# Performance work log

Hardware: AMD Instinct MI355X
Metric: run time of the kernel (lower is better)

## Reference

```python
import jax, jax.numpy as jnp
import numpy as np
import math

K = 32          # knn neighbors
NN = 32         # num_neighbor (kernel columns)
MAP = 32        # map_size
GROUP = 4
IN_C = 64
OUT_C = 64
EPS = 1e-5
TOPK = 3        # neighbors kept per kernel column in topkmax


def knn_idx(xc, k):
    # xc: [B,N,3]; returns indices of k nearest points (self included first)
    sq = -jnp.sum(xc * xc, axis=-1, keepdims=True)            # [B,N,1]
    pair = sq + 2.0 * jnp.einsum('bnd,bmd->bnm', xc, xc) + jnp.swapaxes(sq, 1, 2)
    return jax.lax.top_k(pair, k)[1]                          # [B,N,k]


def topkmax(p):
    # p: [M,k,NN]; keep top-TOPK along neighbor axis (dim=1), softmax over it
    pt = jnp.swapaxes(p, 1, 2)                                # [M,NN,k]
    thr = jax.lax.top_k(pt, TOPK)[0][..., -1:]
    pt = jnp.where(pt >= thr, pt, -1e10)
    return jnp.swapaxes(jax.nn.softmax(pt, axis=-1), 1, 2)


def setup_inputs() -> dict:
    key = jax.random.key(0)
    ks = jax.random.split(key, 8)
    B, N = 8, 2048
    in_c_x = IN_C // 2
    F = IN_C + in_c_x                                         # 96
    return {
        'x': jax.random.normal(ks[0], (B, 3, N), jnp.float32),
        'feature': jax.random.normal(ks[1], (B, IN_C, N), jnp.float32),
        'B_mat': jax.random.normal(ks[2], (7, MAP), jnp.float32),
        'kernels': jax.random.normal(ks[3], (3, NN), jnp.float32),
        'mlp_w': jax.random.normal(ks[4], (in_c_x, 2 * MAP), jnp.float32) * 0.1,
        'mlp_b': jnp.zeros((in_c_x,), jnp.float32),
        'conv_w': jax.random.normal(ks[5], (OUT_C, F * NN), jnp.float32) * 0.02,
        'conv_b': jnp.zeros((OUT_C,), jnp.float32),
        'bn_gamma': jnp.ones((OUT_C,), jnp.float32),
        'bn_beta': jnp.zeros((OUT_C,), jnp.float32),
    }


def reference(x, feature, B_mat, kernels, mlp_w, mlp_b, conv_w, conv_b, bn_gamma, bn_beta):
    bsz, in_c, n = feature.shape
    in_c_x = in_c // 2
    F = in_c + in_c_x
    M = bsz * n

    xc = jnp.swapaxes(x, 1, 2)                                # [B,N,3]
    idx = knn_idx(xc, K)                                      # [B,N,K]
    bix = jnp.arange(bsz)[:, None, None]

    x_neighs = xc[bix, idx].reshape(M, K, 3)                  # gather coords
    x_rep = jnp.broadcast_to(x_neighs[:, :1, :], x_neighs.shape)
    x_rel = x_neighs - x_rep
    x_dis = jnp.linalg.norm(x_rel, axis=-1, keepdims=True)

    # random Fourier features of [center, relative, distance]
    ff = (2.0 * math.pi) * jnp.concatenate([x_rep, x_rel, x_dis], -1) @ B_mat  # [M,K,MAP]
    ff = jnp.concatenate([jnp.sin(ff), jnp.cos(ff)], -1)                        # [M,K,2*MAP]
    x_feats = jnp.einsum('mki,oi->mok', ff, mlp_w) + mlp_b[None, :, None]       # [M,in_c_x,K]

    fN = jnp.swapaxes(feature, 1, 2)                          # [B,N,C]
    feats = fN[bix, idx].reshape(M, K, in_c)                  # gather features
    feats = jnp.swapaxes(feats, 1, 2)                         # [M,C,K]
    feats = jnp.concatenate([feats, x_feats], axis=1)         # [M,F,K]

    one_pad = jnp.zeros((K, NN), feature.dtype).at[0, 0].set(1.0)
    perm = topkmax(jnp.einsum('mkd,dn->mkn', x_rel, kernels) + one_pad)  # [M,K,NN]

    # group channel shuffle (F > 3 + in_c_x holds for in_c=64)
    feats = feats.reshape(M, GROUP, F // GROUP, K).transpose(0, 2, 1, 3).reshape(M, F, K)
    feats = jnp.einsum('mfk,mkn->mfn', feats, perm).reshape(M, F * NN)

    out = (feats @ conv_w.T + conv_b).reshape(bsz, n, -1)
    out = jnp.swapaxes(out, 1, 2)                             # [B,out_c,N]

    # BatchNorm1d, training-mode batch statistics over (B,N)
    mean = out.mean(axis=(0, 2), keepdims=True)
    var = out.var(axis=(0, 2), keepdims=True)
    return bn_gamma[None, :, None] * (out - mean) / jnp.sqrt(var + EPS) + bn_beta[None, :, None]
```

## Files before the change

kernel.cpp:

```cpp
#include <hip/hip_runtime.h>
#include <hip/hip_bf16.h>
#include <math.h>

#define NPTS 2048
#define NBATCH 8
#define MTOT (NBATCH*NPTS)
#define KROW 4096
#define OUTC 64

using bf16x8 = __attribute__((ext_vector_type(8))) short;
using f32x4  = __attribute__((ext_vector_type(4))) float;

__device__ __forceinline__ unsigned short f2bf(float f) {
    unsigned u = __float_as_uint(f);
    unsigned r = u + 0x7FFFu + ((u >> 16) & 1u);
    return (unsigned short)(r >> 16);
}
__device__ __forceinline__ unsigned pk2bf(float lo, float hi) {
    __hip_bfloat162 h2 = __float22bfloat162_rn(make_float2(lo, hi));
    return *reinterpret_cast<unsigned*>(&h2);
}

__device__ __forceinline__ unsigned wave_max_u32(unsigned v) {
    int x = (int)v, t;
    t = __builtin_amdgcn_update_dpp(x, x, 0x111, 0xF, 0xF, false); x = ((unsigned)t > (unsigned)x) ? t : x;
    t = __builtin_amdgcn_update_dpp(x, x, 0x112, 0xF, 0xF, false); x = ((unsigned)t > (unsigned)x) ? t : x;
    t = __builtin_amdgcn_update_dpp(x, x, 0x114, 0xF, 0xF, false); x = ((unsigned)t > (unsigned)x) ? t : x;
    t = __builtin_amdgcn_update_dpp(x, x, 0x118, 0xF, 0xF, false); x = ((unsigned)t > (unsigned)x) ? t : x;
    t = __builtin_amdgcn_update_dpp(x, x, 0x142, 0xa, 0xF, false); x = ((unsigned)t > (unsigned)x) ? t : x;
    t = __builtin_amdgcn_update_dpp(x, x, 0x143, 0xc, 0xF, false); x = ((unsigned)t > (unsigned)x) ? t : x;
    return (unsigned)__builtin_amdgcn_readlane(x, 63);
}

__global__ __launch_bounds__(512, 4) void knn_kernel(const float* __restrict__ x,
                                                     int* __restrict__ idxout) {
    __shared__ float4 ps[NPTS];
    int t = threadIdx.x;
    int b = blockIdx.x / (NPTS / 8);
    int grp = blockIdx.x % (NPTS / 8);
    const float* xb = x + (size_t)b * 3 * NPTS;
    for (int i = t; i < NPTS; i += 512) {
        float vx = xb[i], vy = xb[NPTS + i], vz = xb[2 * NPTS + i];
        ps[i] = make_float4(vx, vy, vz, -((vx * vx + vy * vy) + vz * vz));
    }
    __syncthreads();
    int wave = t >> 6, lane = t & 63;
    int n = grp * 8 + wave;
    float4 pc = ps[n];
    float cx = pc.x, cy = pc.y, cz = pc.z;
    float sqn = pc.w;
    float cx2 = 2.0f * cx, cy2 = 2.0f * cy, cz2 = 2.0f * cz;

    unsigned key[32];
#pragma unroll
    for (int j = 0; j < 32; j++) {
        int cand = j * 64 + lane;
        float4 q = ps[cand];
        float v = sqn + q.w;
        v = fmaf(cx2, q.x, v);
        v = fmaf(cy2, q.y, v);
        v = fmaf(cz2, q.z, v);
        unsigned u = __float_as_uint(v);
        unsigned ord = u ^ ((u >> 31) ? 0xFFFFFFFFu : 0x80000000u);
        key[j] = (ord & 0xFFFFFFE0u) | (unsigned)j;
    }
#pragma unroll
    for (int k = 2; k <= 32; k <<= 1) {
#pragma unroll
        for (int j = k >> 1; j >= 1; j >>= 1) {
#pragma unroll
            for (int i = 0; i < 32; i++) {
                int l2 = i ^ j;
                if (l2 > i) {
                    unsigned a = key[i], bb = key[l2];
                    unsigned hi = a > bb ? a : bb, lo = a > bb ? bb : a;
                    if ((i & k) == 0) { key[i] = hi; key[l2] = lo; }
                    else              { key[i] = lo; key[l2] = hi; }
                }
            }
        }
    }
    int sg = 0;
    for (int r = 0; r < 40; r++) {
        unsigned m = wave_max_u32(key[0]);
        unsigned long long ball = __ballot(key[0] == m);
        int bl = __ffsll(ball) - 1;
        int gidx = (int)(m & 31u) * 64 + bl;
        if (lane == r) sg = gidx;
        bool won = (lane == bl);
#pragma unroll
        for (int i = 0; i < 11; i++) key[i] = won ? key[i + 1] : key[i];
        key[11] = won ? 0u : key[11];
    }
    double cxd = (double)cx, cyd = (double)cy, czd = (double)cz;
    double sqnd = -((cxd * cxd + cyd * cyd) + czd * czd);
    double v; int oid;
    if (lane < 40) {
        float4 qq = ps[sg];
        double mx = (double)qq.x, my = (double)qq.y, mz = (double)qq.z;
        double dot = (cxd * mx + cyd * my) + czd * mz;
        double sqm = -((mx * mx + my * my) + mz * mz);
        v = (sqnd + 2.0 * dot) + sqm;
        oid = sg;
    } else {
        v = -1.0e300; oid = (1 << 28) + lane;
    }
#pragma unroll
    for (int k = 2; k <= 64; k <<= 1) {
#pragma unroll
        for (int j = k >> 1; j >= 1; j >>= 1) {
            double ov = __shfl_xor(v, j);
            int oi = __shfl_xor(oid, j);
            bool amLow = (lane & j) == 0;
            bool asc = (lane & k) == 0;
            bool gt = (ov > v) || (ov == v && oi < oid);
            bool ga = gt != amLow;
            bool take = asc ? ga : !ga;
            if (take) { v = ov; oid = oi; }
        }
    }
    if (lane >= 32) idxout[((size_t)b * NPTS + n) * 32 + (63 - lane)] = oid;
}

__global__ __launch_bounds__(256) void transpose_kernel(const float* __restrict__ feat,
                                                        unsigned short* __restrict__ fTb) {
    __shared__ float tile[64][65];
    int b = blockIdx.x / 32;
    int n0 = (blockIdx.x % 32) * 64;
    int t = threadIdx.x;
    int nt = t % 64, cg = t / 64;
    for (int cc = 0; cc < 16; cc++) {
        int c2 = cg * 16 + cc;
        tile[c2][nt] = feat[((size_t)b * 64 + c2) * NPTS + n0 + nt];
    }
    __syncthreads();
    int c2 = t % 64, ng = t / 64;
    for (int nn2 = 0; nn2 < 16; nn2++) {
        int n = ng * 16 + nn2;
        fTb[((size_t)b * NPTS + n0 + n) * 64 + c2] = f2bf(tile[c2][n]);
    }
}

__global__ __launch_bounds__(256) void wprep2_kernel(
    const float* __restrict__ cw, const float* __restrict__ mlpw,
    const float* __restrict__ mb, const float* __restrict__ cb,
    unsigned short* __restrict__ WtT, float* __restrict__ cbw) {
    int oc = blockIdx.x;
    int t = threadIdx.x;
    for (int i = t; i < 2048; i += 256) {
        int f = i >> 5, col = i & 31;
        int r = (f % 24) * 4 + f / 24;
        WtT[(size_t)oc * KROW + i] = f2bf(cw[(size_t)oc * 3072 + r * 32 + col]);
    }
    for (int i = t; i < 2048; i += 256) {
        int j = i >> 5, col = i & 31;
        float s = 0.f;
        for (int o2 = 0; o2 < 32; o2++) {
            int f = 64 + o2;
            int r = (f % 24) * 4 + f / 24;
            s = fmaf(mlpw[o2 * 64 + j], cw[(size_t)oc * 3072 + r * 32 + col], s);
        }
        WtT[(size_t)oc * KROW + 2048 + i] = f2bf(s);
    }
    if (t == 0) {
        float s = cb[oc];
        for (int o2 = 0; o2 < 32; o2++) {
            int f = 64 + o2;
            int r = (f % 24) * 4 + f / 24;
            float rowsum = 0.f;
            for (int col = 0; col < 32; col++) rowsum += cw[(size_t)oc * 3072 + r * 32 + col];
            s = fmaf(mb[o2], rowsum, s);
        }
        cbw[oc] = s;
    }
}

__global__ void kprep_kernel(const float* __restrict__ ker, double* __restrict__ kerd) {
    int i = threadIdx.x;
    if (i < 96) kerd[i] = (double)ker[i];
}

__global__ __launch_bounds__(256) void perm_kernel(
    const float* __restrict__ x, const int* __restrict__ idx,
    const double* __restrict__ kerd, unsigned short* __restrict__ PTws) {
    int t = threadIdx.x;
    int wv = t >> 6, l = t & 63;
    int c = l & 31;
    int cbase = l & 32;
    int m = blockIdx.x * 8 + wv * 2 + (l >> 5);
    int b = m >> 11;
    int ik = idx[(size_t)m * 32 + c];
    const float* xb = x + (size_t)b * 3 * NPTS;
    float nx0 = xb[ik], ny0 = xb[NPTS + ik], nz0 = xb[2 * NPTS + ik];
    float cx = __shfl(nx0, cbase), cy = __shfl(ny0, cbase), cz = __shfl(nz0, cbase);
    double rxd = (double)nx0 - (double)cx;
    double ryd = (double)ny0 - (double)cy;
    double rzd = (double)nz0 - (double)cz;
    double ck0 = kerd[c], ck1 = kerd[32 + c], ck2 = kerd[64 + c];

    double pd[32];
#pragma unroll
    for (int kk = 0; kk < 32; kk++) {
        double bx = __shfl(rxd, cbase + kk);
        double by = __shfl(ryd, cbase + kk);
        double bz = __shfl(rzd, cbase + kk);
        pd[kk] = bx * ck0 + by * ck1 + bz * ck2;
    }
    if (c == 0) pd[0] += 1.0;

    double m1 = -1.0e300, m2 = -1.0e300, m3 = -1.0e300;
#pragma unroll
    for (int kk = 0; kk < 32; kk++) {
        double v = pd[kk];
        double t2 = fmin(v, m1);
        double t3 = fmin(v, m2);
        m1 = fmax(m1, v);
        m2 = fmax(m2, t2);
        m3 = fmax(m3, t3);
    }
    float pv[32];
    float ssum = 0.f;
#pragma unroll
    for (int kk = 0; kk < 32; kk++) {
        float e = (pd[kk] >= m3) ? __expf((float)(pd[kk] - m1)) : 0.f;
        pv[kk] = e; ssum += e;
    }
    float rs = 1.f / ssum;
#pragma unroll
    for (int kk = 0; kk < 32; kk++) pv[kk] *= rs;

    unsigned w[16];
#pragma unroll
    for (int i = 0; i < 16; i++)
        w[i] = pk2bf(pv[2 * i], pv[2 * i + 1]);
    size_t obase = (size_t)m * 1024 + (size_t)c * 32;
    *(uint4*)&PTws[obase]      = make_uint4(w[0], w[1], w[2], w[3]);
    *(uint4*)&PTws[obase + 8]  = make_uint4(w[4], w[5], w[6], w[7]);
    *(uint4*)&PTws[obase + 16] = make_uint4(w[8], w[9], w[10], w[11]);
    *(uint4*)&PTws[obase + 24] = make_uint4(w[12], w[13], w[14], w[15]);
}

__global__ __launch_bounds__(256) void point3_kernel(
    const float* __restrict__ x, const unsigned short* __restrict__ fTb,
    const int* __restrict__ idx, const float* __restrict__ Bm,
    const unsigned short* __restrict__ PTws, unsigned short* __restrict__ Aof,
    int m_base, int m_count) {
    __shared__ __align__(16) unsigned short lds2[4 * 2560];
    int t = threadIdx.x;
    int wv = t >> 6, l = t & 63;
    int k = l & 31, h = l >> 5;
    unsigned short* G2 = lds2 + wv * 2560;
    int lr = l & 15, lq = l >> 4;
    int gw = blockIdx.x * 4 + wv;
    int nw = gridDim.x * 4;

    for (int mi = gw; mi < m_count; mi += nw) {
        int m = m_base + mi;
        int b = m >> 11;
        int ik = idx[(size_t)m * 32 + k];
        const float* xb = x + (size_t)b * 3 * NPTS;
        float nx0 = xb[ik], ny0 = xb[NPTS + ik], nz0 = xb[2 * NPTS + ik];
        const unsigned short* fr = fTb + (((size_t)b * NPTS + ik) * 64 + h * 32);
        uint4 f0 = *(const uint4*)fr;
        uint4 f1 = *(const uint4*)(fr + 8);
        uint4 f2 = *(const uint4*)(fr + 16);
        uint4 f3 = *(const uint4*)(fr + 24);
        const unsigned short* ptp = PTws + (size_t)m * 1024;
        bf16x8 af0 = *(const bf16x8*)&ptp[lr * 32 + lq * 8];
        bf16x8 af1 = *(const bf16x8*)&ptp[(16 + lr) * 32 + lq * 8];

        float cx = __shfl(nx0, 0), cy = __shfl(ny0, 0), cz = __shfl(nz0, 0);
        float rx = nx0 - cx, ry = ny0 - cy, rz = nz0 - cz;
        float dist = sqrtf((rx * rx + ry * ry) + rz * rz);

        {
            unsigned fw[16] = {f0.x, f0.y, f0.z, f0.w, f1.x, f1.y, f1.z, f1.w,
                               f2.x, f2.y, f2.z, f2.w, f3.x, f3.y, f3.z, f3.w};
#pragma unroll
            for (int c2 = 0; c2 < 16; c2++) {
                unsigned v = fw[c2];
                unsigned o = (unsigned)__shfl_xor((int)v, 1);
                unsigned wr = (k & 1) ? ((o >> 16) | (v & 0xFFFF0000u))
                                      : ((v & 0xFFFFu) | (o << 16));
                int ch = h * 32 + 2 * c2 + (k & 1);
                *(unsigned*)&G2[ch * 40 + (k & ~1)] = wr;
            }
        }
        asm volatile("" ::: "memory");

        size_t obase = (size_t)mi * KROW;
#pragma unroll
        for (int fb = 0; fb < 4; fb++) {
            int row = fb * 16 + lr;
            bf16x8 bfr = *(const bf16x8*)&G2[row * 40 + lq * 8];
            f32x4 d0 = __builtin_amdgcn_mfma_f32_16x16x32_bf16(af0, bfr, (f32x4){0.f, 0.f, 0.f, 0.f}, 0, 0, 0);
            f32x4 d1 = __builtin_amdgcn_mfma_f32_16x16x32_bf16(af1, bfr, (f32x4){0.f, 0.f, 0.f, 0.f}, 0, 0, 0);
            *(uint2*)&Aof[obase + row * 32 + lq * 4] =
                make_uint2(pk2bf(d0.x, d0.y), pk2bf(d0.z, d0.w));
            *(uint2*)&Aof[obase + row * 32 + 16 + lq * 4] =
                make_uint2(pk2bf(d1.x, d1.y), pk2bf(d1.z, d1.w));
        }
        asm volatile("" ::: "memory");

        {
            float u[32];
#pragma unroll
            for (int f = 0; f < 32; f++) {
                float uu = cx * Bm[f];
                uu = fmaf(cy, Bm[32 + f], uu);
                uu = fmaf(cz, Bm[64 + f], uu);
                uu = fmaf(rx, Bm[96 + f], uu);
                uu = fmaf(ry, Bm[128 + f], uu);
                uu = fmaf(rz, Bm[160 + f], uu);
                uu = fmaf(dist, Bm[192 + f], uu);
                u[f] = 6.28318530717958647692f * uu;
            }
            float tv[32];
            if (h == 0) {
#pragma unroll
                for (int f = 0; f < 32; f++) tv[f] = __sinf(u[f]);
            } else {
#pragma unroll
                for (int f = 0; f < 32; f++) tv[f] = __cosf(u[f]);
            }
#pragma unroll
            for (int jj = 0; jj < 16; jj++) {
                float o0 = __shfl_xor(tv[jj], 1);
                float o1 = __shfl_xor(tv[jj + 16], 1);
                float lo = (k & 1) ? o1 : tv[jj];
                float hi = (k & 1) ? tv[jj + 16] : o0;
                unsigned wr = pk2bf(lo, hi);
                int row = h * 32 + (k & 1) * 16 + jj;
                *(unsigned*)&G2[row * 40 + (k & ~1)] = wr;
            }
        }
        asm volatile("" ::: "memory");

#pragma unroll
        for (int fb = 0; fb < 4; fb++) {
            int row = fb * 16 + lr;
            bf16x8 bfr = *(const bf16x8*)&G2[row * 40 + lq * 8];
            f32x4 d0 = __builtin_amdgcn_mfma_f32_16x16x32_bf16(af0, bfr, (f32x4){0.f, 0.f, 0.f, 0.f}, 0, 0, 0);
            f32x4 d1 = __builtin_amdgcn_mfma_f32_16x16x32_bf16(af1, bfr, (f32x4){0.f, 0.f, 0.f, 0.f}, 0, 0, 0);
            int f = 64 + row;
            *(uint2*)&Aof[obase + f * 32 + lq * 4] =
                make_uint2(pk2bf(d0.x, d0.y), pk2bf(d0.z, d0.w));
            *(uint2*)&Aof[obase + f * 32 + 16 + lq * 4] =
                make_uint2(pk2bf(d1.x, d1.y), pk2bf(d1.z, d1.w));
        }
        asm volatile("" ::: "memory");
    }
}

__global__ __launch_bounds__(256) void conv2_kernel(
    const unsigned short* __restrict__ A, const unsigned short* __restrict__ WtT,
    const float* __restrict__ cbw, float* __restrict__ outp, int m_base) {
    __shared__ unsigned short Al[64 * 72];
    __shared__ unsigned short Wl[64 * 72];
    int t = threadIdx.x;
    int wv = t >> 6, l = t & 63;
    int lr = l & 15, lq = l >> 4;
    int m0 = blockIdx.x * 64;
    int mr = t >> 3, kq = t & 7;
    f32x4 acc[4] = {};
    for (int ks = 0; ks < 64; ks++) {
        int k0 = ks * 64;
        uint4 a0 = *(const uint4*)&A[(size_t)(m0 + mr) * KROW + k0 + kq * 8];
        uint4 a1 = *(const uint4*)&A[(size_t)(m0 + mr + 32) * KROW + k0 + kq * 8];
        uint4 w0 = *(const uint4*)&WtT[(size_t)mr * KROW + k0 + kq * 8];
        uint4 w1 = *(const uint4*)&WtT[(size_t)(mr + 32) * KROW + k0 + kq * 8];
        __syncthreads();
        *(uint4*)&Al[mr * 72 + kq * 8] = a0;
        *(uint4*)&Al[(mr + 32) * 72 + kq * 8] = a1;
        *(uint4*)&Wl[mr * 72 + kq * 8] = w0;
        *(uint4*)&Wl[(mr + 32) * 72 + kq * 8] = w1;
        __syncthreads();
#pragma unroll
        for (int kk = 0; kk < 2; kk++) {
            bf16x8 af = *(const bf16x8*)&Al[(wv * 16 + lr) * 72 + kk * 32 + lq * 8];
#pragma unroll
            for (int ocb = 0; ocb < 4; ocb++) {
                bf16x8 wf = *(const bf16x8*)&Wl[(ocb * 16 + lr) * 72 + kk * 32 + lq * 8];
                acc[ocb] = __builtin_amdgcn_mfma_f32_16x16x32_bf16(af, wf, acc[ocb], 0, 0, 0);
            }
        }
    }
    int m = m_base + m0 + wv * 16 + lq * 4;
    int b = m >> 11, n = m & 2047;
#pragma unroll
    for (int ocb = 0; ocb < 4; ocb++) {
        int oc = ocb * 16 + lr;
        float bias = cbw[oc];
        float4 v = make_float4(acc[ocb].x + bias, acc[ocb].y + bias,
                               acc[ocb].z + bias, acc[ocb].w + bias);
        *(float4*)&outp[((size_t)(b * 64 + oc)) * 2048 + n] = v;
    }
}

__global__ __launch_bounds__(256) void bn1_kernel(const float* __restrict__ outp,
                                                  float* __restrict__ sums) {
    int c = blockIdx.x, t = threadIdx.x;
    float s = 0.0f, s2 = 0.0f;
    for (int b = 0; b < NBATCH; b++) {
        const float* p = outp + ((size_t)b * 64 + c) * NPTS;
        for (int i = t; i < NPTS; i += 256) {
            float v = p[i];
            s += v; s2 = fmaf(v, v, s2);
        }
    }
    __shared__ float r1[256], r2[256];
    r1[t] = s; r2[t] = s2;
    __syncthreads();
    for (int st = 128; st > 0; st >>= 1) {
        if (t < st) { r1[t] += r1[t + st]; r2[t] += r2[t + st]; }
        __syncthreads();
    }
    if (t == 0) { sums[c] = r1[0]; sums[64 + c] = r2[0]; }
}

__global__ __launch_bounds__(256) void bn2_kernel(float* __restrict__ outp,
                                                  const float* __restrict__ sums,
                                                  const float* __restrict__ gamma,
                                                  const float* __restrict__ beta) {
    int i = blockIdx.x * 256 + threadIdx.x;
    if (i >= MTOT * 64) return;
    int c = (i >> 11) & 63;
    float mean = sums[c] * (1.0f / (float)MTOT);
    float var = sums[64 + c] * (1.0f / (float)MTOT) - mean * mean;
    float inv = rsqrtf(var + 1e-5f);
    outp[i] = fmaf(gamma[c], (outp[i] - mean) * inv, beta[c]);
}

extern "C" void kernel_launch(void* const* d_in, const int* in_sizes, int n_in,
                              void* d_out, int out_size, void* d_ws, size_t ws_size,
                              hipStream_t stream) {
    (void)in_sizes; (void)n_in; (void)out_size;
    const float* x    = (const float*)d_in[0];
    const float* fea  = (const float*)d_in[1];
    const float* Bm   = (const float*)d_in[2];
    const float* ker  = (const float*)d_in[3];
    const float* mw   = (const float*)d_in[4];
    const float* mb   = (const float*)d_in[5];
    const float* cw   = (const float*)d_in[6];
    const float* cb   = (const float*)d_in[7];
    const float* gam  = (const float*)d_in[8];
    const float* bet  = (const float*)d_in[9];
    float* outp = (float*)d_out;

    char* wsb = (char*)d_ws;
    size_t off = 0;
    auto carve = [&](size_t sz) {
        void* p = wsb + off;
        off = (off + sz + 255) & ~(size_t)255;
        return p;
    };
    unsigned short* fTb  = (unsigned short*)carve((size_t)MTOT * 64 * 2);
    int*            idxw = (int*)carve((size_t)MTOT * 32 * 4);
    unsigned short* WtT  = (unsigned short*)carve((size_t)OUTC * KROW * 2);
    float*          cbw  = (float*)carve(64 * 4);
    double*         kerd = (double*)carve(96 * 8);
    float*          sums = (float*)carve(2 * 64 * 4);
    unsigned short* PTws = (unsigned short*)carve((size_t)MTOT * 1024 * 2);
    size_t fixedEnd = off;
    int CS = 16384;
    while (fixedEnd + (size_t)CS * KROW * 2 > ws_size && CS > 2048) CS >>= 1;
    unsigned short* Aof = (unsigned short*)(wsb + fixedEnd);

    knn_kernel<<<NBATCH * (NPTS / 8), 512, 0, stream>>>(x, idxw);
    transpose_kernel<<<NBATCH * 32, 256, 0, stream>>>(fea, fTb);
    wprep2_kernel<<<64, 256, 0, stream>>>(cw, mw, mb, cb, WtT, cbw);
    kprep_kernel<<<1, 128, 0, stream>>>(ker, kerd);
    perm_kernel<<<MTOT / 8, 256, 0, stream>>>(x, idxw, kerd, PTws);

    for (int c0 = 0; c0 < MTOT; c0 += CS) {
        point3_kernel<<<1536, 256, 0, stream>>>(x, fTb, idxw, Bm, PTws, Aof, c0, CS);
        conv2_kernel<<<CS / 64, 256, 0, stream>>>(Aof, WtT, cbw, outp, c0);
    }
    bn1_kernel<<<64, 256, 0, stream>>>(outp, sums);
    bn2_kernel<<<(MTOT * 64 + 255) / 256, 256, 0, stream>>>(outp, sums, gam, bet);
}
```

Baseline: 203.7 us.

## Double-buffer conv GEMM, halve M tile, fuse BN statistics via atomics

Measured after the change: 187.6 us. -7.9%, faster.

```diff
diff --git a/kernel.cpp b/kernel.cpp
--- a/kernel.cpp
+++ b/kernel.cpp
@@ -352,70 +352,76 @@
     }
 }
 
-__global__ __launch_bounds__(256) void conv2_kernel(
+__global__ __launch_bounds__(256) void conv3_kernel(
     const unsigned short* __restrict__ A, const unsigned short* __restrict__ WtT,
-    const float* __restrict__ cbw, float* __restrict__ outp, int m_base) {
-    __shared__ unsigned short Al[64 * 72];
-    __shared__ unsigned short Wl[64 * 72];
+    const float* __restrict__ cbw, float* __restrict__ outp,
+    float* __restrict__ sums, int m_base) {
+    __shared__ unsigned short Al[2][32 * 72];
+    __shared__ unsigned short Wl[2][64 * 72];
+    __shared__ float bnred[128];
     int t = threadIdx.x;
     int wv = t >> 6, l = t & 63;
     int lr = l & 15, lq = l >> 4;
-    int m0 = blockIdx.x * 64;
-    int mr = t >> 3, kq = t & 7;
-    f32x4 acc[4] = {};
+    int m0 = blockIdx.x * 32;
+    int ar = t >> 3, kq = t & 7;
+    int mh = wv >> 1, oh = wv & 1;
+    if (t < 128) bnred[t] = 0.f;
+    f32x4 acc[2] = {};
+    {
+        uint4 a0 = *(const uint4*)&A[(size_t)(m0 + ar) * KROW + kq * 8];
+        uint4 w0 = *(const uint4*)&WtT[(size_t)ar * KROW + kq * 8];
+        uint4 w1 = *(const uint4*)&WtT[(size_t)(ar + 32) * KROW + kq * 8];
+        *(uint4*)&Al[0][ar * 72 + kq * 8] = a0;
+        *(uint4*)&Wl[0][ar * 72 + kq * 8] = w0;
+        *(uint4*)&Wl[0][(ar + 32) * 72 + kq * 8] = w1;
+    }
+    __syncthreads();
+    int cur = 0;
     for (int ks = 0; ks < 64; ks++) {
-        int k0 = ks * 64;
-        uint4 a0 = *(const uint4*)&A[(size_t)(m0 + mr) * KROW + k0 + kq * 8];
-        uint4 a1 = *(const uint4*)&A[(size_t)(m0 + mr + 32) * KROW + k0 + kq * 8];
-        uint4 w0 = *(const uint4*)&WtT[(size_t)mr * KROW + k0 + kq * 8];
-        uint4 w1 = *(const uint4*)&WtT[(size_t)(mr + 32) * KROW + k0 + kq * 8];
-        __syncthreads();
-        *(uint4*)&Al[mr * 72 + kq * 8] = a0;
-        *(uint4*)&Al[(mr + 32) * 72 + kq * 8] = a1;
-        *(uint4*)&Wl[mr * 72 + kq * 8] = w0;
-        *(uint4*)&Wl[(mr + 32) * 72 + kq * 8] = w1;
-        __syncthreads();
+        uint4 na0, nw0, nw1;
+        bool pf = ks < 63;
+        if (pf) {
+            int k0 = (ks + 1) * 64;
+            na0 = *(const uint4*)&A[(size_t)(m0 + ar) * KROW + k0 + kq * 8];
+            nw0 = *(const uint4*)&WtT[(size_t)ar * KROW + k0 + kq * 8];
+            nw1 = *(const uint4*)&WtT[(size_t)(ar + 32) * KROW + k0 + kq * 8];
+        }
 #pragma unroll
         for (int kk = 0; kk < 2; kk++) {
-            bf16x8 af = *(const bf16x8*)&Al[(wv * 16 + lr) * 72 + kk * 32 + lq * 8];
-#pragma unroll
-            for (int ocb = 0; ocb < 4; ocb++) {
-                bf16x8 wf = *(const bf16x8*)&Wl[(ocb * 16 + lr) * 72 + kk * 32 + lq * 8];
+            bf16x8 af = *(const bf16x8*)&Al[cur][(mh * 16 + lr) * 72 + kk * 32 + lq * 8];
+#pragma unroll
+            for (int ocb = 0; ocb < 2; ocb++) {
+                bf16x8 wf = *(const bf16x8*)&Wl[cur][(oh * 32 + ocb * 16 + lr) * 72 + kk * 32 + lq * 8];
                 acc[ocb] = __builtin_amdgcn_mfma_f32_16x16x32_bf16(af, wf, acc[ocb], 0, 0, 0);
             }
         }
-    }
-    int m = m_base + m0 + wv * 16 + lq * 4;
+        if (pf) {
+            *(uint4*)&Al[cur ^ 1][ar * 72 + kq * 8] = na0;
+            *(uint4*)&Wl[cur ^ 1][ar * 72 + kq * 8] = nw0;
+            *(uint4*)&Wl[cur ^ 1][(ar + 32) * 72 + kq * 8] = nw1;
+            __syncthreads();
+            cur ^= 1;
+        }
+    }
+    int m = m_base + m0 + mh * 16 + lq * 4;
     int b = m >> 11, n = m & 2047;
 #pragma unroll
-    for (int ocb = 0; ocb < 4; ocb++) {
-        int oc = ocb * 16 + lr;
+    for (int ocb = 0; ocb < 2; ocb++) {
+        int oc = oh * 32 + ocb * 16 + lr;
         float bias = cbw[oc];
         float4 v = make_float4(acc[ocb].x + bias, acc[ocb].y + bias,
                                acc[ocb].z + bias, acc[ocb].w + bias);
         *(float4*)&outp[((size_t)(b * 64 + oc)) * 2048 + n] = v;
-    }
-}
-
-__global__ __launch_bounds__(256) void bn1_kernel(const float* __restrict__ outp,
-                                                  float* __restrict__ sums) {
-    int c = blockIdx.x, t = threadIdx.x;
-    float s = 0.0f, s2 = 0.0f;
-    for (int b = 0; b < NBATCH; b++) {
-        const float* p = outp + ((size_t)b * 64 + c) * NPTS;
-        for (int i = t; i < NPTS; i += 256) {
-            float v = p[i];
-            s += v; s2 = fmaf(v, v, s2);
-        }
-    }
-    __shared__ float r1[256], r2[256];
-    r1[t] = s; r2[t] = s2;
+        float s = (v.x + v.y) + (v.z + v.w);
+        float s2 = fmaf(v.x, v.x, fmaf(v.y, v.y, fmaf(v.z, v.z, v.w * v.w)));
+        atomicAdd(&bnred[oc * 2], s);
+        atomicAdd(&bnred[oc * 2 + 1], s2);
+    }
     __syncthreads();
-    for (int st = 128; st > 0; st >>= 1) {
-        if (t < st) { r1[t] += r1[t + st]; r2[t] += r2[t + st]; }
-        __syncthreads();
-    }
-    if (t == 0) { sums[c] = r1[0]; sums[64 + c] = r2[0]; }
+    if (t < 64) {
+        atomicAdd(&sums[t], bnred[t * 2]);
+        atomicAdd(&sums[64 + t], bnred[t * 2 + 1]);
+    }
 }
 
 __global__ __launch_bounds__(256) void bn2_kernel(float* __restrict__ outp,
@@ -466,6 +472,7 @@
     while (fixedEnd + (size_t)CS * KROW * 2 > ws_size && CS > 2048) CS >>= 1;
     unsigned short* Aof = (unsigned short*)(wsb + fixedEnd);
 
+    hipMemsetAsync(sums, 0, 2 * 64 * 4, stream);
     knn_kernel<<<NBATCH * (NPTS / 8), 512, 0, stream>>>(x, idxw);
     transpose_kernel<<<NBATCH * 32, 256, 0, stream>>>(fea, fTb);
     wprep2_kernel<<<64, 256, 0, stream>>>(cw, mw, mb, cb, WtT, cbw);
@@ -474,8 +481,7 @@
 
     for (int c0 = 0; c0 < MTOT; c0 += CS) {
         point3_kernel<<<1536, 256, 0, stream>>>(x, fTb, idxw, Bm, PTws, Aof, c0, CS);
-        conv2_kernel<<<CS / 64, 256, 0, stream>>>(Aof, WtT, cbw, outp, c0);
-    }
-    bn1_kernel<<<64, 256, 0, stream>>>(outp, sums);
+        conv3_kernel<<<CS / 32, 256, 0, stream>>>(Aof, WtT, cbw, outp, sums, c0);
+    }
     bn2_kernel<<<(MTOT * 64 + 255) / 256, 256, 0, stream>>>(outp, sums, gam, bet);
 }
```
